# Performance work log

Hardware: AMD Instinct MI355X
Metric: run time of the kernel (lower is better)

## Reference

```python
import math
import jax, jax.numpy as jnp
import numpy as np

NUM_HEADS = 8
FACTOR = 5


def setup_inputs() -> dict:
    key = jax.random.key(0)
    ks = jax.random.split(key, 5)
    B, S, D = 8, 2048, 512
    s = 1.0 / math.sqrt(D)
    return {
        "x": jax.random.normal(ks[0], (B, S, D), dtype=jnp.float32),
        "wq": jax.random.normal(ks[1], (D, D), dtype=jnp.float32) * s,
        "bq": jnp.zeros((D,), jnp.float32),
        "wk": jax.random.normal(ks[2], (D, D), dtype=jnp.float32) * s,
        "bk": jnp.zeros((D,), jnp.float32),
        "wv": jax.random.normal(ks[3], (D, D), dtype=jnp.float32) * s,
        "bv": jnp.zeros((D,), jnp.float32),
        "wo": jax.random.normal(ks[4], (D, D), dtype=jnp.float32) * s,
        "bo": jnp.zeros((D,), jnp.float32),
    }


def reference(x, wq, bq, wk, bk, wv, bv, wo, bo):
    B, S, Dm = x.shape
    H = NUM_HEADS
    Dh = Dm // H
    scale = jnp.sqrt(jnp.float32(Dh))
    # u = min(factor * ceil(ln(S)), S); S is static so compute in Python
    u = min(FACTOR * int(math.ceil(math.log(S))), S)

    def split_heads(t):  # [B,S,Dm] -> [B,H,S,Dh]
        return t.reshape(B, S, H, Dh).transpose(0, 2, 1, 3)

    q = split_heads(x @ wq + bq)
    k = split_heads(x @ wk + bk)
    v = split_heads(x @ wv + bv)

    # S >= 64 -> sparse branch (static decision).
    # Full logits only to compute sparsity measure M (max - mean over keys).
    logits = jnp.einsum("bhqd,bhkd->bhqk", q, k) / scale  # [B,H,S,S]
    M = jnp.max(logits, axis=-1) - jnp.mean(logits, axis=-1)  # [B,H,S]
    _, top_idx = jax.lax.top_k(M, u)  # [B,H,u]

    # Gather top-u queries and run dense attention only for them.
    q_top = jnp.take_along_axis(q, top_idx[..., None], axis=2)  # [B,H,u,Dh]
    top_logits = jnp.einsum("bhqd,bhkd->bhqk", q_top, k) / scale  # [B,H,u,S]
    top_w = jax.nn.softmax(top_logits, axis=-1)
    top_out = jnp.einsum("bhqk,bhkd->bhqd", top_w, v)  # [B,H,u,Dh]

    # Non-selected queries get the mean of V; scatter top outputs in.
    out = jnp.broadcast_to(jnp.mean(v, axis=2, keepdims=True), v.shape)
    b_idx = jnp.arange(B)[:, None, None]
    h_idx = jnp.arange(H)[None, :, None]
    out = out.at[b_idx, h_idx, top_idx].set(top_out)  # [B,H,S,Dh]

    out = out.transpose(0, 2, 1, 3).reshape(B, S, Dm)
    return out @ wo + bo
```

## Files before the change

kernel.cpp:

```cpp
#include <hip/hip_runtime.h>
#include <hip/hip_bf16.h>
#include <math.h>

#define NB 8
#define NS 2048
#define ND 512
#define NH 8
#define DHD 64
#define NU 40
#define NBH 64
#define NM 16384

typedef __attribute__((ext_vector_type(8))) short short8;
typedef __attribute__((ext_vector_type(4))) short short4v;
typedef __attribute__((ext_vector_type(4))) float f32x4;

__device__ __forceinline__ short f2bf(float f) {
  __hip_bfloat16 h = __float2bfloat16(f);
  return *reinterpret_cast<short*>(&h);
}
__device__ __forceinline__ float bf2f(short s) {
  __hip_bfloat16 h;
  *reinterpret_cast<short*>(&h) = s;
  return __bfloat162float(h);
}

__device__ __forceinline__ void gload_lds16(const short* g, short* l) {
  __builtin_amdgcn_global_load_lds(
      (const __attribute__((address_space(1))) unsigned int*)g,
      (__attribute__((address_space(3))) unsigned int*)l, 16, 0, 0);
}

__global__ void prep(const float* __restrict__ x, const float* __restrict__ w0,
                     const float* __restrict__ w1, const float* __restrict__ w2,
                     short* __restrict__ Xs, short* __restrict__ Wts) {
  if (blockIdx.x < 8192) {
    int i = blockIdx.x * 256 + threadIdx.x;
    const float4 v = *(const float4*)(x + (size_t)i * 4);
    int row = i >> 7;
    int col = (i & 127) << 2;
    float vv[4] = {v.x, v.y, v.z, v.w};
    short4v hi, lo;
#pragma unroll
    for (int j = 0; j < 4; ++j) {
      short h = f2bf(vv[j]);
      hi[j] = h;
      lo[j] = f2bf(vv[j] - bf2f(h));
    }
    *(short4v*)(Xs + (size_t)row * 1024 + col) = hi;
    *(short4v*)(Xs + (size_t)row * 1024 + 512 + col) = lo;
  } else {
    int bw = blockIdx.x - 8192;
    int y = bw >> 8;
    int bxy = bw & 255;
    const float* W = y == 0 ? w0 : y == 1 ? w1 : w2;
    short* dst = Wts + (size_t)y * 512 * 1024;
    __shared__ float tile[32][33];
    int bx = bxy & 15, by = bxy >> 4;
    int k0 = bx * 32, n0 = by * 32;
    int r = threadIdx.x >> 3, cg = (threadIdx.x & 7) * 4;
    const float4 v = *(const float4*)(W + (size_t)(k0 + r) * 512 + n0 + cg);
    tile[r][cg] = v.x; tile[r][cg + 1] = v.y; tile[r][cg + 2] = v.z; tile[r][cg + 3] = v.w;
    __syncthreads();
#pragma unroll
    for (int j = 0; j < 4; ++j) {
      int kk = cg + j;
      float f = tile[kk][r];
      short h = f2bf(f);
      dst[(size_t)(n0 + r) * 1024 + k0 + kk] = h;
      dst[(size_t)(n0 + r) * 1024 + 512 + k0 + kk] = f2bf(f - bf2f(h));
    }
  }
}

__global__ __launch_bounds__(256, 2) void qkvgemm(
    const short* __restrict__ A, const short* __restrict__ Wts,
    const float* __restrict__ bq, const float* __restrict__ bk,
    const float* __restrict__ bv, short* __restrict__ Qs,
    short* __restrict__ Ks, short* __restrict__ Vs) {
  __shared__ short As[2][128][64];
  __shared__ short Bs[2][128][64];
  const int bid = blockIdx.x;
  const int wgid = (bid & 7) * 192 + (bid >> 3);
  const int mb = wgid / 12, y = wgid % 12;
  const int m0 = mb * 128;
  const int wsel = y >> 2;
  const int n0 = (y & 3) * 128;
  const short* Wb = Wts + (size_t)wsel * 512 * 1024;
  const float* bias = wsel == 0 ? bq : wsel == 1 ? bk : bv;
  short* dstbase = wsel == 0 ? Qs : wsel == 1 ? Ks : Vs;

  const int tid = threadIdx.x;
  const int w = tid >> 6, lane = tid & 63;
  const int wm = (w >> 1) * 64, wn = (w & 1) * 64;
  const int fr = lane & 15, fk = lane >> 4;

  f32x4 acc[4][4];
  const f32x4 zz = {0.f, 0.f, 0.f, 0.f};
#pragma unroll
  for (int i = 0; i < 4; ++i)
#pragma unroll
    for (int j = 0; j < 4; ++j) acc[i][j] = zz;

  auto stage = [&](int buf, int kt) {
#pragma unroll
    for (int p = 0; p < 4; ++p) {
      int idx = (p * 4 + w) * 64 + lane;
      int r = idx >> 3, c = idx & 7;
      int cs = c ^ (r & 7);
      int sc = (cs < 4) ? (kt + cs * 8) : (512 + kt + (cs - 4) * 8);
      short* lA = &As[buf][0][0] + (p * 4 + w) * 512;
      short* lB = &Bs[buf][0][0] + (p * 4 + w) * 512;
      gload_lds16(A + (size_t)(m0 + r) * 1024 + sc, lA);
      gload_lds16(Wb + (size_t)(n0 + r) * 1024 + sc, lB);
    }
  };

  stage(0, 0);
  __syncthreads();
  for (int kt = 0; kt < 512; kt += 32) {
    int cur = (kt >> 5) & 1;
    if (kt + 32 < 512) stage(cur ^ 1, kt + 32);
    short8 ah[4], al[4], bh[4], bl[4];
#pragma unroll
    for (int mf = 0; mf < 4; ++mf) {
      int r = wm + mf * 16 + fr;
      ah[mf] = *(const short8*)&As[cur][r][(fk ^ (r & 7)) << 3];
      al[mf] = *(const short8*)&As[cur][r][((4 + fk) ^ (r & 7)) << 3];
    }
#pragma unroll
    for (int nf = 0; nf < 4; ++nf) {
      int r = wn + nf * 16 + fr;
      bh[nf] = *(const short8*)&Bs[cur][r][(fk ^ (r & 7)) << 3];
      bl[nf] = *(const short8*)&Bs[cur][r][((4 + fk) ^ (r & 7)) << 3];
    }
#pragma unroll
    for (int mf = 0; mf < 4; ++mf)
#pragma unroll
      for (int nf = 0; nf < 4; ++nf) {
        acc[mf][nf] = __builtin_amdgcn_mfma_f32_16x16x32_bf16(bh[nf], ah[mf], acc[mf][nf], 0, 0, 0);
        acc[mf][nf] = __builtin_amdgcn_mfma_f32_16x16x32_bf16(bh[nf], al[mf], acc[mf][nf], 0, 0, 0);
        acc[mf][nf] = __builtin_amdgcn_mfma_f32_16x16x32_bf16(bl[nf], ah[mf], acc[mf][nf], 0, 0, 0);
      }
    __syncthreads();
  }

#pragma unroll
  for (int mf = 0; mf < 4; ++mf) {
    int m = m0 + wm + mf * 16 + fr;
    int b = m >> 11, s = m & 2047;
#pragma unroll
    for (int nf = 0; nf < 4; ++nf) {
      int nb = n0 + wn + nf * 16 + fk * 4;
      float4 bi4 = *(const float4*)(bias + nb);
      int h = nb >> 6, dh = nb & 63;
      short* dst = dstbase + ((size_t)((b << 3) + h) * 2048 + s) * 128;
      short4v hi, lo;
      float bb[4] = {bi4.x, bi4.y, bi4.z, bi4.w};
#pragma unroll
      for (int j = 0; j < 4; ++j) {
        float v = acc[mf][nf][j] + bb[j];
        short hs = f2bf(v);
        hi[j] = hs;
        lo[j] = f2bf(v - bf2f(hs));
      }
      *(short4v*)(dst + dh) = hi;
      *(short4v*)(dst + 64 + dh) = lo;
    }
  }
}

__global__ __launch_bounds__(256) void colmeans(const short* __restrict__ K,
                                                const short* __restrict__ V,
                                                float* __restrict__ kbarf,
                                                float* __restrict__ vbarf) {
  const int bh = blockIdx.x >> 2, part = blockIdx.x & 3;
  const int c = threadIdx.x & 15;
  const int g = threadIdx.x >> 4;
  const int s0 = part * 512 + g * 32;
  const short* Kb = K + (size_t)bh * 2048 * 128;
  const short* Vb = V + (size_t)bh * 2048 * 128;
  float sk[8], sv[8];
#pragma unroll
  for (int e = 0; e < 8; ++e) { sk[e] = 0.f; sv[e] = 0.f; }
  for (int s = s0; s < s0 + 32; ++s) {
    short8 k8 = *(const short8*)(Kb + (size_t)s * 128 + c * 8);
    short8 v8 = *(const short8*)(Vb + (size_t)s * 128 + c * 8);
#pragma unroll
    for (int e = 0; e < 8; ++e) { sk[e] += bf2f(k8[e]); sv[e] += bf2f(v8[e]); }
  }
  __shared__ float rk[16][128], rv[16][128];
#pragma unroll
  for (int e = 0; e < 8; ++e) { rk[g][c * 8 + e] = sk[e]; rv[g][c * 8 + e] = sv[e]; }
  __syncthreads();
  if (threadIdx.x < 64) {
    int d = threadIdx.x;
    float a = 0.f, b2 = 0.f;
    for (int g2 = 0; g2 < 16; ++g2) {
      a += rk[g2][d] + rk[g2][64 + d];
      b2 += rv[g2][d] + rv[g2][64 + d];
    }
    atomicAdd(kbarf + bh * 64 + d, a * (1.f / 2048.f));
    atomicAdd(vbarf + bh * 64 + d, b2 * (1.f / 2048.f));
  }
}

__global__ __launch_bounds__(256, 2) void qkmax(const short* __restrict__ Qs,
                                                const short* __restrict__ Ks,
                                                const float* __restrict__ kbarf,
                                                float* __restrict__ Mval) {
  __shared__ short Kt[2][128][128];
  __shared__ float red[256];
  const int bid = blockIdx.x;
  const int wgid = (bid & 7) * 64 + (bid >> 3);
  const int bh = wgid >> 3, q0 = (wgid & 7) * 256;
  const short* Qb = Qs + ((size_t)bh * 2048 + q0) * 128;
  const short* Kb = Ks + (size_t)bh * 2048 * 128;
  const int tid = threadIdx.x, w = tid >> 6, lane = tid & 63;
  const int fr = lane & 15, fk = lane >> 4;

  short8 qf[4][2][2];
#pragma unroll
  for (int mf = 0; mf < 4; ++mf) {
    int row = w * 64 + mf * 16 + fr;
#pragma unroll
    for (int h = 0; h < 2; ++h)
#pragma unroll
      for (int k0 = 0; k0 < 2; ++k0) {
        int ch = h * 8 + k0 * 4 + fk;
        qf[mf][h][k0] = *(const short8*)(Qb + (size_t)row * 128 + ch * 8);
      }
  }

  f32x4 rmax[4];
  const f32x4 neg = {-1e30f, -1e30f, -1e30f, -1e30f};
#pragma unroll
  for (int mf = 0; mf < 4; ++mf) rmax[mf] = neg;
  const f32x4 zz = {0.f, 0.f, 0.f, 0.f};

  auto stageK = [&](int buf, int t) {
#pragma unroll
    for (int p = 0; p < 8; ++p) {
      int idx = (p * 4 + w) * 64 + lane;
      int r = idx >> 4, c = idx & 15;
      int cs = c ^ (r & 15);
      short* lb = &Kt[buf][0][0] + (p * 4 + w) * 512;
      gload_lds16(Kb + (size_t)(t * 128 + r) * 128 + cs * 8, lb);
    }
  };

  stageK(0, 0);
  __syncthreads();
  for (int t = 0; t < 16; ++t) {
    int cur = t & 1;
    if (t < 15) stageK(cur ^ 1, t + 1);
#pragma unroll
    for (int nf = 0; nf < 8; ++nf) {
      int r = nf * 16 + fr;
      short8 kfh[2], kfl[2];
#pragma unroll
      for (int k0 = 0; k0 < 2; ++k0) {
        kfh[k0] = *(const short8*)&Kt[cur][r][((k0 * 4 + fk) ^ (r & 15)) << 3];
        kfl[k0] = *(const short8*)&Kt[cur][r][((8 + k0 * 4 + fk) ^ (r & 15)) << 3];
      }
#pragma unroll
      for (int mf = 0; mf < 4; ++mf) {
        f32x4 a = zz;
#pragma unroll
        for (int k0 = 0; k0 < 2; ++k0) {
          a = __builtin_amdgcn_mfma_f32_16x16x32_bf16(qf[mf][0][k0], kfh[k0], a, 0, 0, 0);
          a = __builtin_amdgcn_mfma_f32_16x16x32_bf16(qf[mf][0][k0], kfl[k0], a, 0, 0, 0);
          a = __builtin_amdgcn_mfma_f32_16x16x32_bf16(qf[mf][1][k0], kfh[k0], a, 0, 0, 0);
        }
#pragma unroll
        for (int j = 0; j < 4; ++j) rmax[mf][j] = fmaxf(rmax[mf][j], a[j]);
      }
    }
    __syncthreads();
  }

#pragma unroll
  for (int mf = 0; mf < 4; ++mf)
#pragma unroll
    for (int j = 0; j < 4; ++j) {
      float r = rmax[mf][j];
      r = fmaxf(r, __shfl_xor(r, 1, 64));
      r = fmaxf(r, __shfl_xor(r, 2, 64));
      r = fmaxf(r, __shfl_xor(r, 4, 64));
      r = fmaxf(r, __shfl_xor(r, 8, 64));
      if (fr == 0) red[w * 64 + mf * 16 + fk * 4 + j] = r;
    }
  __syncthreads();

  {
    const short* qp = Qs + ((size_t)bh * 2048 + q0 + tid) * 128;
    const float* kb = kbarf + bh * 64;
    float dot = 0.f;
#pragma unroll
    for (int ch = 0; ch < 8; ++ch) {
      short8 hi = *(const short8*)(qp + ch * 8);
      short8 lo = *(const short8*)(qp + 64 + ch * 8);
#pragma unroll
      for (int e = 0; e < 8; ++e) dot += (bf2f(hi[e]) + bf2f(lo[e])) * kb[ch * 8 + e];
    }
    Mval[(size_t)bh * 2048 + q0 + tid] = (red[tid] - dot) * 0.125f;
  }
}

__global__ __launch_bounds__(256) void topk40(const float* __restrict__ Mval,
                                              int* __restrict__ tidx) {
  __shared__ float vals[4][32][64];
  const int w = threadIdx.x >> 6, lane = threadIdx.x & 63;
  const int bh = blockIdx.x * 4 + w;
  const float* src = Mval + (size_t)bh * 2048;
#pragma unroll
  for (int j = 0; j < 32; ++j) vals[w][j][lane] = src[j * 64 + lane];

  for (int it = 0; it < NU; ++it) {
    float best = -INFINITY;
    int bi = 1 << 30;
#pragma unroll
    for (int j = 0; j < 32; ++j) {
      float x = vals[w][j][lane];
      int idx = j * 64 + lane;
      if (x > best) { best = x; bi = idx; }
    }
#pragma unroll
    for (int off = 1; off < 64; off <<= 1) {
      float ov = __shfl_xor(best, off, 64);
      int oi = __shfl_xor(bi, off, 64);
      if (ov > best || (ov == best && oi < bi)) { best = ov; bi = oi; }
    }
    if (lane == 0) tidx[bh * NU + it] = bi;
    if ((bi & 63) == lane) vals[w][bi >> 6][lane] = -INFINITY;
  }
}

__global__ __launch_bounds__(256) void topattn1(const short* __restrict__ Qs,
                                                const short* __restrict__ Ks,
                                                const short* __restrict__ Vs,
                                                const int* __restrict__ topidx,
                                                float* __restrict__ pacc,
                                                float* __restrict__ pm,
                                                float* __restrict__ pl) {
  __shared__ float qs[40][68];
  __shared__ float Kst[64][132];
  __shared__ float Vsh[128][68];
  __shared__ float st[40][132];
  __shared__ float m_s[40], l_s[40], r_s[40];
  __shared__ int tix[40];
  const int tid = threadIdx.x;
  const int bh = blockIdx.x, kc = blockIdx.y;
  const short* Kb = Ks + (size_t)bh * 2048 * 128;
  const short* Vb = Vs + (size_t)bh * 2048 * 128;

  if (tid < 40) {
    tix[tid] = topidx[bh * NU + tid];
    m_s[tid] = -INFINITY;
    l_s[tid] = 0.f;
  }
  __syncthreads();
  for (int i = tid; i < 40 * 64; i += 256) {
    int q = i >> 6, dd2 = i & 63;
    const short* qp = Qs + ((size_t)bh * 2048 + tix[q]) * 128;
    qs[q][dd2] = bf2f(qp[dd2]) + bf2f(qp[64 + dd2]);
  }
  const int tx = tid & 31, ty = tid >> 5;
  const int d = tid & 63, qb = tid >> 6;
  float acc[10];
#pragma unroll
  for (int j = 0; j < 10; ++j) acc[j] = 0.f;
  __syncthreads();

  for (int t = 0; t < 4; ++t) {
    int krow0 = kc * 512 + t * 128;
#pragma unroll
    for (int p = 0; p < 4; ++p) {
      int idx = tid + (p << 8);
      int r = idx >> 3, cg = (idx & 7) << 3;
      const short8 kh = *(const short8*)(Kb + (size_t)(krow0 + r) * 128 + cg);
      const short8 kl = *(const short8*)(Kb + (size_t)(krow0 + r) * 128 + 64 + cg);
      const short8 vh = *(const short8*)(Vb + (size_t)(krow0 + r) * 128 + cg);
      const short8 vl = *(const short8*)(Vb + (size_t)(krow0 + r) * 128 + 64 + cg);
#pragma unroll
      for (int j = 0; j < 8; ++j) {
        Kst[cg + j][r] = bf2f(kh[j]) + bf2f(kl[j]);
        Vsh[r][cg + j] = bf2f(vh[j]) + bf2f(vl[j]);
      }
    }
    __syncthreads();

    {
      float c5[5][4];
#pragma unroll
      for (int i = 0; i < 5; ++i)
#pragma unroll
        for (int j = 0; j < 4; ++j) c5[i][j] = 0.f;
      for (int dd = 0; dd < 64; ++dd) {
        const float4 b4 = *(const float4*)&Kst[dd][tx << 2];
#pragma unroll
        for (int i = 0; i < 5; ++i) {
          float a = qs[ty * 5 + i][dd];
          c5[i][0] = fmaf(a, b4.x, c5[i][0]);
          c5[i][1] = fmaf(a, b4.y, c5[i][1]);
          c5[i][2] = fmaf(a, b4.z, c5[i][2]);
          c5[i][3] = fmaf(a, b4.w, c5[i][3]);
        }
      }
#pragma unroll
      for (int i = 0; i < 5; ++i) {
        float4 o;
        o.x = c5[i][0] * 0.125f; o.y = c5[i][1] * 0.125f;
        o.z = c5[i][2] * 0.125f; o.w = c5[i][3] * 0.125f;
        *(float4*)&st[ty * 5 + i][tx << 2] = o;
      }
    }
    __syncthreads();

    if (tid < 160) {
      int q = tid >> 2, sub = tid & 3;
      float tm = -INFINITY;
#pragma unroll
      for (int kk = 0; kk < 32; ++kk) tm = fmaxf(tm, st[q][sub * 32 + kk]);
      tm = fmaxf(tm, __shfl_xor(tm, 1, 64));
      tm = fmaxf(tm, __shfl_xor(tm, 2, 64));
      float mold = m_s[q];
      float mnew = fmaxf(mold, tm);
      float sum = 0.f;
#pragma unroll
      for (int kk = 0; kk < 32; ++kk) {
        float ww = __expf(st[q][sub * 32 + kk] - mnew);
        st[q][sub * 32 + kk] = ww;
        sum += ww;
      }
      sum += __shfl_xor(sum, 1, 64);
      sum += __shfl_xor(sum, 2, 64);
      if (sub == 0) {
        float r = __expf(mold - mnew);
        l_s[q] = l_s[q] * r + sum;
        m_s[q] = mnew;
        r_s[q] = r;
      }
    }
    __syncthreads();

#pragma unroll
    for (int j = 0; j < 10; ++j) {
      int q = qb + (j << 2);
      float a = 0.f;
#pragma unroll
      for (int kk = 0; kk < 128; kk += 4) {
        float4 ww = *(const float4*)&st[q][kk];
        a = fmaf(ww.x, Vsh[kk + 0][d], a);
        a = fmaf(ww.y, Vsh[kk + 1][d], a);
        a = fmaf(ww.z, Vsh[kk + 2][d], a);
        a = fmaf(ww.w, Vsh[kk + 3][d], a);
      }
      acc[j] = acc[j] * r_s[q] + a;
    }
    __syncthreads();
  }

  int pcb = bh * 4 + kc;
#pragma unroll
  for (int j = 0; j < 10; ++j) {
    int q = qb + (j << 2);
    pacc[((size_t)pcb * NU + q) * 64 + d] = acc[j];
  }
  if (tid < 40) {
    pm[pcb * NU + tid] = m_s[tid];
    pl[pcb * NU + tid] = l_s[tid];
  }
}

__global__ __launch_bounds__(256) void topcombine(const float* __restrict__ pacc,
                                                  const float* __restrict__ pm,
                                                  const float* __restrict__ pl,
                                                  float* __restrict__ tout,
                                                  const float* __restrict__ vbarf,
                                                  const float* __restrict__ Wo,
                                                  const float* __restrict__ bo,
                                                  float* __restrict__ om) {
  if (blockIdx.x < 64) {
    const int bh = blockIdx.x;
    const int d = threadIdx.x & 63, qb = threadIdx.x >> 6;
#pragma unroll
    for (int j = 0; j < 10; ++j) {
      int q = qb + (j << 2);
      float m0 = pm[(bh * 4 + 0) * NU + q], m1 = pm[(bh * 4 + 1) * NU + q];
      float m2 = pm[(bh * 4 + 2) * NU + q], m3 = pm[(bh * 4 + 3) * NU + q];
      float mx = fmaxf(fmaxf(m0, m1), fmaxf(m2, m3));
      float e0 = __expf(m0 - mx), e1 = __expf(m1 - mx);
      float e2 = __expf(m2 - mx), e3 = __expf(m3 - mx);
      float L = pl[(bh * 4 + 0) * NU + q] * e0 + pl[(bh * 4 + 1) * NU + q] * e1 +
                pl[(bh * 4 + 2) * NU + q] * e2 + pl[(bh * 4 + 3) * NU + q] * e3;
      float o = (pacc[((size_t)(bh * 4 + 0) * NU + q) * 64 + d] * e0 +
                 pacc[((size_t)(bh * 4 + 1) * NU + q) * 64 + d] * e1 +
                 pacc[((size_t)(bh * 4 + 2) * NU + q) * 64 + d] * e2 +
                 pacc[((size_t)(bh * 4 + 3) * NU + q) * 64 + d] * e3) / L;
      tout[((size_t)bh * NU + q) * 64 + d] = o;
    }
  } else {
    __shared__ float mred[4][64];
    int blk2 = blockIdx.x - 64;
    int b = blk2 >> 3, n0 = (blk2 & 7) * 64;
    int n = n0 + (threadIdx.x & 63), kq = threadIdx.x >> 6;
    const float* vb = vbarf + b * 512;
    float acc = 0.f;
#pragma unroll 8
    for (int k = kq * 128; k < kq * 128 + 128; ++k)
      acc = fmaf(vb[k], Wo[(size_t)k * 512 + n], acc);
    mred[kq][threadIdx.x & 63] = acc;
    __syncthreads();
    if (kq == 0)
      om[b * 512 + n] = bo[n] + mred[0][n - n0] + mred[1][n - n0] +
                        mred[2][n - n0] + mred[3][n - n0];
  }
}

__global__ void fillout(const float* __restrict__ om, float* __restrict__ out) {
  const size_t n4 = (size_t)NM * 128;
  for (size_t i = (size_t)blockIdx.x * 256 + threadIdx.x; i < n4;
       i += (size_t)gridDim.x * 256) {
    int m = (int)(i >> 7), c4 = (int)(i & 127) << 2;
    int b = m >> 11;
    *(float4*)(out + (size_t)m * 512 + c4) = *(const float4*)(om + b * 512 + c4);
  }
}

__global__ __launch_bounds__(256) void deltaout(const float* __restrict__ tout,
                                                const float* __restrict__ vbarf,
                                                const int* __restrict__ tidx,
                                                const float* __restrict__ Wo,
                                                float* __restrict__ out) {
  const int g = blockIdx.x;
  const int bh = g / 40;
  const int b = bh >> 3, h = bh & 7;
  const int s = tidx[g];
  __shared__ float dsh[64];
  if (threadIdx.x < 64)
    dsh[threadIdx.x] = tout[(size_t)g * 64 + threadIdx.x] - vbarf[bh * 64 + threadIdx.x];
  __syncthreads();
  const int n = threadIdx.x;
  float a0 = 0.f, a1 = 0.f;
#pragma unroll 8
  for (int dh = 0; dh < 64; ++dh) {
    float d = dsh[dh];
    const float* wrow = Wo + (size_t)(h * 64 + dh) * 512;
    a0 = fmaf(d, wrow[n], a0);
    a1 = fmaf(d, wrow[n + 256], a1);
  }
  float* orow = out + ((size_t)b * 2048 + s) * 512;
  atomicAdd(orow + n, a0);
  atomicAdd(orow + n + 256, a1);
}

extern "C" void kernel_launch(void* const* d_in, const int* in_sizes, int n_in,
                              void* d_out, int out_size, void* d_ws, size_t ws_size,
                              hipStream_t stream) {
  (void)in_sizes; (void)n_in; (void)out_size; (void)ws_size;
  const float* x  = (const float*)d_in[0];
  const float* wq = (const float*)d_in[1];
  const float* bq = (const float*)d_in[2];
  const float* wk = (const float*)d_in[3];
  const float* bk = (const float*)d_in[4];
  const float* wv = (const float*)d_in[5];
  const float* bv = (const float*)d_in[6];
  const float* wo = (const float*)d_in[7];
  const float* bo = (const float*)d_in[8];
  float* out = (float*)d_out;

  short* Xs   = (short*)d_ws;
  short* Wts  = Xs + (size_t)16384 * 1024;
  short* Qsb  = Wts + (size_t)3 * 512 * 1024;
  short* Ksb  = Qsb + (size_t)NBH * NS * 128;
  short* Vsb  = Ksb + (size_t)NBH * NS * 128;
  float* Mval = (float*)(Vsb + (size_t)NBH * NS * 128);
  float* kbarf = Mval + (size_t)NBH * NS;
  float* vbarf = kbarf + NBH * 64;
  int* tidx   = (int*)(vbarf + NBH * 64);
  float* pacc = (float*)(tidx + NBH * NU);
  float* pm   = pacc + (size_t)NBH * 4 * NU * 64;
  float* pl   = pm + NBH * 4 * NU;
  float* tout = pl + NBH * 4 * NU;
  float* om   = tout + (size_t)NBH * NU * 64;

  hipMemsetAsync(kbarf, 0, 2 * NBH * 64 * sizeof(float), stream);
  prep<<<8960, 256, 0, stream>>>(x, wq, wk, wv, Xs, Wts);
  qkvgemm<<<1536, 256, 0, stream>>>(Xs, Wts, bq, bk, bv, Qsb, Ksb, Vsb);
  colmeans<<<NBH * 4, 256, 0, stream>>>(Ksb, Vsb, kbarf, vbarf);
  qkmax<<<512, 256, 0, stream>>>(Qsb, Ksb, kbarf, Mval);
  topk40<<<16, 256, 0, stream>>>(Mval, tidx);
  topattn1<<<dim3(NBH, 4), 256, 0, stream>>>(Qsb, Ksb, Vsb, tidx, pacc, pm, pl);
  topcombine<<<128, 256, 0, stream>>>(pacc, pm, pl, tout, vbarf, wo, bo, om);
  fillout<<<2048, 256, 0, stream>>>(om, out);
  deltaout<<<NBH * NU, 256, 0, stream>>>(tout, vbarf, tidx, wo, out);
}
```

Before: 338.4 us.

## Deepen GEMM/qkmax prefetch, use 32x32 MFMA, fuse output fill with delta scatter

The QKV GEMM and qkmax loops switch to a two-ahead prefetch that waits on explicit vmcnt counts, raises wave priority around the MFMA block, and uses raw barriers. qkmax also moves from 16x16x32 to 32x32x16 bf16 MFMA tiles with a re-mapped row-max reduction. topk now writes a per-row slot map, and fillout plus the atomic deltaout are merged into one outall kernel. outall writes each output row once and adds the Wo-projected deltas for the selected heads, removing the atomics. The costs are an extra 512 KB memset and a full 16384-block output pass that reads slot8 for every row.

```diff
diff --git a/kernel.cpp b/kernel.cpp
--- a/kernel.cpp
+++ b/kernel.cpp
@@ -14,6 +14,7 @@
 typedef __attribute__((ext_vector_type(8))) short short8;
 typedef __attribute__((ext_vector_type(4))) short short4v;
 typedef __attribute__((ext_vector_type(4))) float f32x4;
+typedef __attribute__((ext_vector_type(16))) float f32x16;
 
 __device__ __forceinline__ short f2bf(float f) {
   __hip_bfloat16 h = __float2bfloat16(f);
@@ -102,7 +103,8 @@
 #pragma unroll
     for (int j = 0; j < 4; ++j) acc[i][j] = zz;
 
-  auto stage = [&](int buf, int kt) {
+  auto stage = [&](int buf, int t) {
+    const int kt = t * 32;
 #pragma unroll
     for (int p = 0; p < 4; ++p) {
       int idx = (p * 4 + w) * 64 + lane;
@@ -117,10 +119,16 @@
   };
 
   stage(0, 0);
-  __syncthreads();
-  for (int kt = 0; kt < 512; kt += 32) {
-    int cur = (kt >> 5) & 1;
-    if (kt + 32 < 512) stage(cur ^ 1, kt + 32);
+  stage(1, 1);
+  for (int t = 0; t < 16; ++t) {
+    const int cur = t & 1;
+    if (t < 15) {
+      asm volatile("s_waitcnt vmcnt(8)" ::: "memory");
+    } else {
+      asm volatile("s_waitcnt vmcnt(0)" ::: "memory");
+    }
+    __builtin_amdgcn_s_barrier();
+
     short8 ah[4], al[4], bh[4], bl[4];
 #pragma unroll
     for (int mf = 0; mf < 4; ++mf) {
@@ -134,6 +142,7 @@
       bh[nf] = *(const short8*)&Bs[cur][r][(fk ^ (r & 7)) << 3];
       bl[nf] = *(const short8*)&Bs[cur][r][((4 + fk) ^ (r & 7)) << 3];
     }
+    __builtin_amdgcn_s_setprio(1);
 #pragma unroll
     for (int mf = 0; mf < 4; ++mf)
 #pragma unroll
@@ -142,7 +151,10 @@
         acc[mf][nf] = __builtin_amdgcn_mfma_f32_16x16x32_bf16(bh[nf], al[mf], acc[mf][nf], 0, 0, 0);
         acc[mf][nf] = __builtin_amdgcn_mfma_f32_16x16x32_bf16(bl[nf], ah[mf], acc[mf][nf], 0, 0, 0);
       }
-    __syncthreads();
+    __builtin_amdgcn_s_setprio(0);
+    __builtin_amdgcn_sched_barrier(0);
+    __builtin_amdgcn_s_barrier();
+    if (t < 14) stage(cur, t + 2);
   }
 
 #pragma unroll
@@ -217,78 +229,96 @@
   const short* Qb = Qs + ((size_t)bh * 2048 + q0) * 128;
   const short* Kb = Ks + (size_t)bh * 2048 * 128;
   const int tid = threadIdx.x, w = tid >> 6, lane = tid & 63;
-  const int fr = lane & 15, fk = lane >> 4;
-
-  short8 qf[4][2][2];
-#pragma unroll
-  for (int mf = 0; mf < 4; ++mf) {
-    int row = w * 64 + mf * 16 + fr;
-#pragma unroll
-    for (int h = 0; h < 2; ++h)
-#pragma unroll
-      for (int k0 = 0; k0 < 2; ++k0) {
-        int ch = h * 8 + k0 * 4 + fk;
-        qf[mf][h][k0] = *(const short8*)(Qb + (size_t)row * 128 + ch * 8);
-      }
-  }
-
-  f32x4 rmax[4];
-  const f32x4 neg = {-1e30f, -1e30f, -1e30f, -1e30f};
-#pragma unroll
-  for (int mf = 0; mf < 4; ++mf) rmax[mf] = neg;
-  const f32x4 zz = {0.f, 0.f, 0.f, 0.f};
+  const int l31 = lane & 31, khalf = lane >> 5;
+
+  short8 qf[2][2][4];
+#pragma unroll
+  for (int g = 0; g < 2; ++g) {
+    int row = w * 64 + g * 32 + l31;
+#pragma unroll
+    for (int hl = 0; hl < 2; ++hl)
+#pragma unroll
+      for (int kc = 0; kc < 4; ++kc)
+        qf[g][hl][kc] =
+            *(const short8*)(Qb + (size_t)row * 128 + hl * 64 + kc * 16 + khalf * 8);
+  }
+
+  f32x16 rmax[2];
+#pragma unroll
+  for (int g = 0; g < 2; ++g)
+#pragma unroll
+    for (int e = 0; e < 16; ++e) rmax[g][e] = -1e30f;
 
   auto stageK = [&](int buf, int t) {
 #pragma unroll
     for (int p = 0; p < 8; ++p) {
-      int idx = (p * 4 + w) * 64 + lane;
+      int idx = p * 256 + tid;
       int r = idx >> 4, c = idx & 15;
       int cs = c ^ (r & 15);
-      short* lb = &Kt[buf][0][0] + (p * 4 + w) * 512;
+      short* lb = &Kt[buf][0][0] + (size_t)(p * 256 + w * 64) * 8;
       gload_lds16(Kb + (size_t)(t * 128 + r) * 128 + cs * 8, lb);
     }
   };
 
   stageK(0, 0);
-  __syncthreads();
+  stageK(1, 1);
   for (int t = 0; t < 16; ++t) {
-    int cur = t & 1;
-    if (t < 15) stageK(cur ^ 1, t + 1);
-#pragma unroll
-    for (int nf = 0; nf < 8; ++nf) {
-      int r = nf * 16 + fr;
-      short8 kfh[2], kfl[2];
-#pragma unroll
-      for (int k0 = 0; k0 < 2; ++k0) {
-        kfh[k0] = *(const short8*)&Kt[cur][r][((k0 * 4 + fk) ^ (r & 15)) << 3];
-        kfl[k0] = *(const short8*)&Kt[cur][r][((8 + k0 * 4 + fk) ^ (r & 15)) << 3];
-      }
-#pragma unroll
-      for (int mf = 0; mf < 4; ++mf) {
-        f32x4 a = zz;
-#pragma unroll
-        for (int k0 = 0; k0 < 2; ++k0) {
-          a = __builtin_amdgcn_mfma_f32_16x16x32_bf16(qf[mf][0][k0], kfh[k0], a, 0, 0, 0);
-          a = __builtin_amdgcn_mfma_f32_16x16x32_bf16(qf[mf][0][k0], kfl[k0], a, 0, 0, 0);
-          a = __builtin_amdgcn_mfma_f32_16x16x32_bf16(qf[mf][1][k0], kfh[k0], a, 0, 0, 0);
+    const int cur = t & 1;
+    if (t < 15) {
+      asm volatile("s_waitcnt vmcnt(8)" ::: "memory");
+    } else {
+      asm volatile("s_waitcnt vmcnt(0)" ::: "memory");
+    }
+    __builtin_amdgcn_s_barrier();
+
+    __builtin_amdgcn_s_setprio(1);
+#pragma unroll
+    for (int kg = 0; kg < 4; ++kg) {
+      int r = kg * 32 + l31;
+      short8 kfr[2][4];
+#pragma unroll
+      for (int hl = 0; hl < 2; ++hl)
+#pragma unroll
+        for (int kc = 0; kc < 4; ++kc) {
+          int ch = hl * 8 + kc * 2 + khalf;
+          kfr[hl][kc] = *(const short8*)&Kt[cur][r][(ch ^ (r & 15)) << 3];
         }
 #pragma unroll
-        for (int j = 0; j < 4; ++j) rmax[mf][j] = fmaxf(rmax[mf][j], a[j]);
-      }
-    }
-    __syncthreads();
-  }
-
-#pragma unroll
-  for (int mf = 0; mf < 4; ++mf)
-#pragma unroll
-    for (int j = 0; j < 4; ++j) {
-      float r = rmax[mf][j];
+      for (int g = 0; g < 2; ++g) {
+        f32x16 a;
+#pragma unroll
+        for (int e = 0; e < 16; ++e) a[e] = 0.f;
+#pragma unroll
+        for (int kc = 0; kc < 4; ++kc)
+          a = __builtin_amdgcn_mfma_f32_32x32x16_bf16(qf[g][0][kc], kfr[0][kc], a, 0, 0, 0);
+#pragma unroll
+        for (int kc = 0; kc < 4; ++kc)
+          a = __builtin_amdgcn_mfma_f32_32x32x16_bf16(qf[g][0][kc], kfr[1][kc], a, 0, 0, 0);
+#pragma unroll
+        for (int kc = 0; kc < 4; ++kc)
+          a = __builtin_amdgcn_mfma_f32_32x32x16_bf16(qf[g][1][kc], kfr[0][kc], a, 0, 0, 0);
+#pragma unroll
+        for (int e = 0; e < 16; ++e) rmax[g][e] = fmaxf(rmax[g][e], a[e]);
+      }
+    }
+    __builtin_amdgcn_s_setprio(0);
+    __builtin_amdgcn_sched_barrier(0);
+    __builtin_amdgcn_s_barrier();
+    if (t < 14) stageK(cur, t + 2);
+  }
+
+#pragma unroll
+  for (int g = 0; g < 2; ++g)
+#pragma unroll
+    for (int e = 0; e < 16; ++e) {
+      float r = rmax[g][e];
       r = fmaxf(r, __shfl_xor(r, 1, 64));
       r = fmaxf(r, __shfl_xor(r, 2, 64));
       r = fmaxf(r, __shfl_xor(r, 4, 64));
       r = fmaxf(r, __shfl_xor(r, 8, 64));
-      if (fr == 0) red[w * 64 + mf * 16 + fk * 4 + j] = r;
+      r = fmaxf(r, __shfl_xor(r, 16, 64));
+      if (l31 == 0)
+        red[w * 64 + g * 32 + (e & 3) + 8 * (e >> 2) + 4 * khalf] = r;
     }
   __syncthreads();
 
@@ -308,7 +338,8 @@
 }
 
 __global__ __launch_bounds__(256) void topk40(const float* __restrict__ Mval,
-                                              int* __restrict__ tidx) {
+                                              int* __restrict__ tidx,
+                                              int* __restrict__ slot8) {
   __shared__ float vals[4][32][64];
   const int w = threadIdx.x >> 6, lane = threadIdx.x & 63;
   const int bh = blockIdx.x * 4 + w;
@@ -331,7 +362,10 @@
       int oi = __shfl_xor(bi, off, 64);
       if (ov > best || (ov == best && oi < bi)) { best = ov; bi = oi; }
     }
-    if (lane == 0) tidx[bh * NU + it] = bi;
+    if (lane == 0) {
+      tidx[bh * NU + it] = bi;
+      slot8[((size_t)(bh >> 3) * 2048 + bi) * 8 + (bh & 7)] = it;
+    }
     if ((bi & 63) == lane) vals[w][bi >> 6][lane] = -INFINITY;
   }
 }
@@ -518,41 +552,38 @@
   }
 }
 
-__global__ void fillout(const float* __restrict__ om, float* __restrict__ out) {
-  const size_t n4 = (size_t)NM * 128;
-  for (size_t i = (size_t)blockIdx.x * 256 + threadIdx.x; i < n4;
-       i += (size_t)gridDim.x * 256) {
-    int m = (int)(i >> 7), c4 = (int)(i & 127) << 2;
-    int b = m >> 11;
-    *(float4*)(out + (size_t)m * 512 + c4) = *(const float4*)(om + b * 512 + c4);
-  }
-}
-
-__global__ __launch_bounds__(256) void deltaout(const float* __restrict__ tout,
-                                                const float* __restrict__ vbarf,
-                                                const int* __restrict__ tidx,
-                                                const float* __restrict__ Wo,
-                                                float* __restrict__ out) {
-  const int g = blockIdx.x;
-  const int bh = g / 40;
-  const int b = bh >> 3, h = bh & 7;
-  const int s = tidx[g];
+__global__ __launch_bounds__(256) void outall(const float* __restrict__ om,
+                                              const int* __restrict__ slot8,
+                                              const float* __restrict__ tout,
+                                              const float* __restrict__ vbarf,
+                                              const float* __restrict__ Wo,
+                                              float* __restrict__ out) {
+  const int r = blockIdx.x;
+  const int b = r >> 11;
+  const int n = threadIdx.x;
+  float o0 = om[b * 512 + n];
+  float o1 = om[b * 512 + n + 256];
   __shared__ float dsh[64];
-  if (threadIdx.x < 64)
-    dsh[threadIdx.x] = tout[(size_t)g * 64 + threadIdx.x] - vbarf[bh * 64 + threadIdx.x];
-  __syncthreads();
-  const int n = threadIdx.x;
-  float a0 = 0.f, a1 = 0.f;
+#pragma unroll
+  for (int h = 0; h < 8; ++h) {
+    int it = slot8[(size_t)r * 8 + h];
+    if (it >= 0) {
+      int bh = b * 8 + h;
+      int g = bh * NU + it;
+      __syncthreads();
+      if (n < 64) dsh[n] = tout[(size_t)g * 64 + n] - vbarf[bh * 64 + n];
+      __syncthreads();
 #pragma unroll 8
-  for (int dh = 0; dh < 64; ++dh) {
-    float d = dsh[dh];
-    const float* wrow = Wo + (size_t)(h * 64 + dh) * 512;
-    a0 = fmaf(d, wrow[n], a0);
-    a1 = fmaf(d, wrow[n + 256], a1);
-  }
-  float* orow = out + ((size_t)b * 2048 + s) * 512;
-  atomicAdd(orow + n, a0);
-  atomicAdd(orow + n + 256, a1);
+      for (int dh = 0; dh < 64; ++dh) {
+        float d = dsh[dh];
+        const float* wrow = Wo + (size_t)(h * 64 + dh) * 512;
+        o0 = fmaf(d, wrow[n], o0);
+        o1 = fmaf(d, wrow[n + 256], o1);
+      }
+    }
+  }
+  out[(size_t)r * 512 + n] = o0;
+  out[(size_t)r * 512 + n + 256] = o1;
 }
 
 extern "C" void kernel_launch(void* const* d_in, const int* in_sizes, int n_in,
@@ -579,20 +610,21 @@
   float* kbarf = Mval + (size_t)NBH * NS;
   float* vbarf = kbarf + NBH * 64;
   int* tidx   = (int*)(vbarf + NBH * 64);
-  float* pacc = (float*)(tidx + NBH * NU);
+  int* slot8  = tidx + NBH * NU;
+  float* pacc = (float*)(slot8 + (size_t)NM * 8);
   float* pm   = pacc + (size_t)NBH * 4 * NU * 64;
   float* pl   = pm + NBH * 4 * NU;
   float* tout = pl + NBH * 4 * NU;
   float* om   = tout + (size_t)NBH * NU * 64;
 
   hipMemsetAsync(kbarf, 0, 2 * NBH * 64 * sizeof(float), stream);
+  hipMemsetAsync(slot8, 0xFF, (size_t)NM * 8 * sizeof(int), stream);
   prep<<<8960, 256, 0, stream>>>(x, wq, wk, wv, Xs, Wts);
   qkvgemm<<<1536, 256, 0, stream>>>(Xs, Wts, bq, bk, bv, Qsb, Ksb, Vsb);
   colmeans<<<NBH * 4, 256, 0, stream>>>(Ksb, Vsb, kbarf, vbarf);
   qkmax<<<512, 256, 0, stream>>>(Qsb, Ksb, kbarf, Mval);
-  topk40<<<16, 256, 0, stream>>>(Mval, tidx);
+  topk40<<<16, 256, 0, stream>>>(Mval, tidx, slot8);
   topattn1<<<dim3(NBH, 4), 256, 0, stream>>>(Qsb, Ksb, Vsb, tidx, pacc, pm, pl);
   topcombine<<<128, 256, 0, stream>>>(pacc, pm, pl, tout, vbarf, wo, bo, om);
-  fillout<<<2048, 256, 0, stream>>>(om, out);
-  deltaout<<<NBH * NU, 256, 0, stream>>>(tout, vbarf, tidx, wo, out);
-}
+  outall<<<NM, 256, 0, stream>>>(om, slot8, tout, vbarf, wo, out);
+}
```

Result: slower. 385.3 us (+13.8%).
